# Performance work log

Measured on AMD Instinct MI355X. Metric: run time of the kernel, lower is better.

The kernel has to match this reference:

```python
import jax, jax.numpy as jnp
import numpy as np

D = 64; T = 128; B = 64; R = 20; SEE = 10; H = 4; C = 4
N = 300000; P = 4000; K = 256


def setup_inputs() -> dict:
    key = jax.random.key(0)
    ks = jax.random.split(key, 24)
    g = lambda k, s: jax.random.normal(k, s, dtype=jnp.float32) * 0.05
    return {
        "prob_id": jax.random.randint(ks[0], (T, B), 0, P),
        "skills": jax.random.randint(ks[1], (T, B, C), 0, K),
        "response": jax.random.randint(ks[2], (T, B), 0, 2),
        "bg_index": jax.random.randint(ks[3], (T, B, R), 0, N),
        "mem_prob_ids": jax.random.randint(ks[4], (N,), 0, P),
        "mem_resp": jax.random.randint(ks[5], (N,), 0, 2),
        "mem_concepts": jax.random.randint(ks[6], (N, C), 0, K),
        "states_mem": g(ks[7], (N, D)),
        "concept_emb": g(ks[8], (K - 1, D)),
        "prob_emb": g(ks[9], (P - 1, D)),
        "W_pred": g(ks[10], (9 * D, 1)), "b_pred": jnp.zeros((1,), jnp.float32),
        "W_ih": g(ks[11], (4 * D, 3 * D)), "W_hh": g(ks[12], (D, 3 * D)),
        "b_ih": jnp.zeros((3 * D,), jnp.float32), "b_hh": jnp.zeros((3 * D,), jnp.float32),
        "W_batch": g(ks[13], (H, 3 * D, D)), "b_batch": jnp.zeros((H, D), jnp.float32),
        "W_bg": g(ks[14], (H, 3 * D, D)), "b_bg": jnp.zeros((H, D), jnp.float32),
        "W_bgint": g(ks[15], (6 * D, 6 * D)), "b_bgint": jnp.zeros((6 * D,), jnp.float32),
        "W_hisint": g(ks[16], (2 * D, 6 * D)), "b_hisint": jnp.zeros((6 * D,), jnp.float32),
        "W_inmap": g(ks[17], (10 * D, 4 * D)), "b_inmap": jnp.zeros((4 * D,), jnp.float32),
        "dir_w": g(ks[18], (2, 1)), "heads_map": g(ks[19], (H, 1)),
    }


def _forward(floats, ints):
    (states_mem, concept_emb, prob_emb, W_pred, b_pred, W_ih, W_hh, b_ih, b_hh,
     W_batch, b_batch, W_bg, b_bg, W_bgint, b_bgint, W_hisint, b_hisint,
     W_inmap, b_inmap, dir_w, heads_map) = floats
    prob_id, skills, response, bg_index, mem_prob_ids, mem_resp, mem_concepts = ints
    f32 = states_mem.dtype
    # embedding tables with zero row 0 (padding id)
    prob_cat = jnp.concatenate([jnp.zeros((1, D), f32), prob_emb], axis=0)
    conc_cat = jnp.concatenate([jnp.zeros((1, D), f32), concept_emb], axis=0)

    def prob_rep(pid, sk):
        pr = prob_cat[pid]                                     # [..., D]
        fsum = jnp.sum((sk != 0).astype(f32), axis=-1)
        div = jnp.where(fsum == 0, 1.0, fsum)[..., None]
        mean = jnp.sum(conc_cat[sk], axis=-2) / div            # masked-mean concept emb
        return jnp.concatenate([mean, pr], axis=-1)            # [..., 2D]

    dw = jax.nn.softmax(dir_w, axis=0)                          # [2,1]
    hm = heads_map[:, 0]                                        # [H]

    def step(carry, xt):
        h, h_buf, resp_buf, v_buf, t = carry
        pid, sk, resp, bgi = xt
        respf = resp.astype(f32)
        v = prob_rep(pid, sk)                                   # [B,2D]
        hidden_v = jnp.concatenate([h, v], axis=-1)             # [B,3D]
        bgi = bgi[:, :SEE]                                      # keep first see_ref refs
        bg_h = states_mem[bgi]                                  # [B,S,D] irregular gather
        bg_v = prob_rep(mem_prob_ids[bgi], mem_concepts[bgi])   # [B,S,2D]
        bg_r = mem_resp[bgi].astype(f32)[..., None]             # [B,S,1]
        all_hv = jnp.concatenate([bg_h, bg_v], axis=-1)         # [B,S,3D]
        bg_ctx = jnp.concatenate([all_hv * bg_r, all_hv * (1.0 - bg_r)], axis=-1)  # [B,S,6D]
        # multi-head attention over retrieved background states
        q = jnp.einsum('bk,hkd->bhd', hidden_v, W_batch) + b_batch[None]
        kk = jnp.einsum('bsk,hkd->bhsd', all_hv, W_bg) + b_bg[None, :, None, :]
        att = jax.nn.softmax(jnp.einsum('bhd,bhsd->bhs', q, kk) / np.sqrt(3.0 * D), axis=-1)
        heads = jnp.einsum('bhs,bsk->bhk', att, bg_ctx)          # [B,H,6D]
        bg_atts = jnp.einsum('bhk,h->bk', heads, hm)             # [B,6D]
        # attention over own history (positions 0..t valid)
        rb = resp_buf.astype(f32)[..., None]                     # [B,T+1,1]
        hr_cat = jnp.concatenate([h_buf * rb, h_buf * (1.0 - rb)], axis=-1)  # [B,T+1,2D]
        sc = jnp.einsum('bk,btk->bt', v, v_buf) / np.sqrt(2.0 * D)
        sc = jnp.where(jnp.arange(T + 1)[None, :] <= t, sc, -1e9)
        his_atts = jnp.einsum('bt,btk->bk', jax.nn.softmax(sc, axis=-1), hr_cat)  # [B,2D]
        peer = (bg_atts @ W_bgint + b_bgint) * dw[0, 0] + (his_atts @ W_hisint + b_hisint) * dw[1, 0]
        prob = (jnp.concatenate([peer, v, h], axis=-1) @ W_pred + b_pred)[:, 0]
        v_resp = jnp.concatenate([v * respf[:, None], v * (1.0 - respf[:, None])], axis=-1)
        gru_in = jnp.concatenate([peer, v_resp], axis=-1) @ W_inmap + b_inmap  # [B,4D]
        # GRU cell (torch GRUCell convention)
        gx = gru_in @ W_ih + b_ih
        gh = h @ W_hh + b_hh
        xr, xz, xn = jnp.split(gx, 3, axis=-1)
        hr, hz, hn = jnp.split(gh, 3, axis=-1)
        r = jax.nn.sigmoid(xr + hr)
        z = jax.nn.sigmoid(xz + hz)
        n = jnp.tanh(xn + r * hn)
        new_h = (1.0 - z) * n + z * h
        h_buf = h_buf.at[:, t + 1].set(new_h)
        resp_buf = resp_buf.at[:, t + 1].set(resp.astype(resp_buf.dtype))
        v_buf = v_buf.at[:, t + 1].set(v)
        return (new_h, h_buf, resp_buf, v_buf, t + 1), prob

    init = (jnp.zeros((B, D), f32), jnp.zeros((B, T + 1, D), f32),
            jnp.zeros((B, T + 1), jnp.int32), jnp.zeros((B, T + 1, 2 * D), f32),
            jnp.int32(0))
    xs = (prob_id, skills, response.astype(jnp.int32), bg_index)
    _, probs = jax.lax.scan(step, init, xs)                      # [T,B]
    return probs.T.reshape(-1)                                   # concat over batch, seq_num=T


def reference(prob_id, skills, response, bg_index, mem_prob_ids, mem_resp, mem_concepts,
              states_mem, concept_emb, prob_emb, W_pred, b_pred, W_ih, W_hh, b_ih, b_hh,
              W_batch, b_batch, W_bg, b_bg, W_bgint, b_bgint, W_hisint, b_hisint,
              W_inmap, b_inmap, dir_w, heads_map):
    floats = (states_mem, concept_emb, prob_emb, W_pred, b_pred, W_ih, W_hh, b_ih, b_hh,
              W_batch, b_batch, W_bg, b_bg, W_bgint, b_bgint, W_hisint, b_hisint,
              W_inmap, b_inmap, dir_w, heads_map)
    ints = (prob_id, skills, response, bg_index, mem_prob_ids, mem_resp, mem_concepts)
    return _forward(floats, ints)
```

## Files before the change

### kernel.cpp

```cpp
#include <hip/hip_runtime.h>
#include <hip/hip_bf16.h>

#define TT 128
#define BB 64
#define DD 64
#define RR 20
#define SEE 10
#define HH 4
#define CC 4
#define NITEM (TT*BB*SEE)
typedef __attribute__((ext_vector_type(8))) short short8;
typedef __attribute__((ext_vector_type(4))) float floatx4;

static __device__ __forceinline__ float wave_sum(float v) {
  v += __shfl_xor(v, 32); v += __shfl_xor(v, 16); v += __shfl_xor(v, 8);
  v += __shfl_xor(v, 4);  v += __shfl_xor(v, 2);  v += __shfl_xor(v, 1);
  return v;
}
static __device__ __forceinline__ float wave_max(float v) {
  v = fmaxf(v, __shfl_xor(v, 32)); v = fmaxf(v, __shfl_xor(v, 16)); v = fmaxf(v, __shfl_xor(v, 8));
  v = fmaxf(v, __shfl_xor(v, 4));  v = fmaxf(v, __shfl_xor(v, 2));  v = fmaxf(v, __shfl_xor(v, 1));
  return v;
}
static __device__ __forceinline__ unsigned short f2bf(float x) {
  __hip_bfloat16 h = __float2bfloat16(x);
  return *reinterpret_cast<unsigned short*>(&h);
}
static __device__ __forceinline__ unsigned int pack2(float lo, float hi) {
  return (unsigned int)f2bf(lo) | ((unsigned int)f2bf(hi) << 16);
}
static __device__ __forceinline__ void ldsbar() {
  asm volatile("s_waitcnt lgkmcnt(0)" ::: "memory");
  __builtin_amdgcn_s_barrier();
  asm volatile("" ::: "memory");
}

__global__ void build_v(const int* __restrict__ prob_id, const int* __restrict__ skills,
                        const float* __restrict__ concept_emb, const float* __restrict__ prob_emb,
                        float* __restrict__ V, float* __restrict__ VT) {
  int tb = blockIdx.x; int t = tb >> 6, b = tb & 63; int d = threadIdx.x;
  int pid = prob_id[tb];
  float pr = pid ? prob_emb[(pid - 1) * 64 + d] : 0.0f;
  int cnt = 0; float sum = 0.0f;
#pragma unroll
  for (int c = 0; c < 4; ++c) {
    int sk = skills[tb * 4 + c];
    if (sk) { ++cnt; sum += concept_emb[(sk - 1) * 64 + d]; }
  }
  float mean = sum / (float)(cnt ? cnt : 1);
  V[tb * 128 + d] = mean;
  V[tb * 128 + 64 + d] = pr;
  VT[b * 16384 + d * 128 + t] = mean;
  VT[b * 16384 + (64 + d) * 128 + t] = pr;
}

__global__ __launch_bounds__(256) void gemm_f32(
    const float* __restrict__ A, const float* __restrict__ B, float* __restrict__ C,
    const float* __restrict__ bias, int M, int N, int K,
    int lda, int ldb, int ldc, long sA, long sB, long sC, float scale) {
  __shared__ __align__(16) float As[64 * 36];
  __shared__ __align__(16) float Bs[32 * 64];
  const float* Ab = A + (long)blockIdx.z * sA;
  const float* Bb = B + (long)blockIdx.z * sB;
  float* Cb = C + (long)blockIdx.z * sC;
  int m0 = blockIdx.y * 64, n0 = blockIdx.x * 64;
  int tid = threadIdx.x;
  int ti = tid & 15, tj = tid >> 4;
  float acc[4][4] = {};
  for (int kc = 0; kc < K; kc += 32) {
#pragma unroll
    for (int p = 0; p < 2; ++p) {
      int q = tid + 256 * p;
      int row = q >> 3, kq = q & 7;
      *(float4*)&As[row * 36 + 4 * kq] = *(const float4*)&Ab[(size_t)(m0 + row) * lda + kc + 4 * kq];
    }
#pragma unroll
    for (int p = 0; p < 2; ++p) {
      int q = tid + 256 * p;
      int k = q >> 4, nq = q & 15;
      *(float4*)&Bs[k * 64 + 4 * nq] = *(const float4*)&Bb[(size_t)(kc + k) * ldb + n0 + 4 * nq];
    }
    __syncthreads();
#pragma unroll
    for (int k4 = 0; k4 < 8; ++k4) {
      float4 av[4], bv[4];
#pragma unroll
      for (int m = 0; m < 4; ++m) av[m] = *(const float4*)&As[(ti + 16 * m) * 36 + 4 * k4];
#pragma unroll
      for (int kk = 0; kk < 4; ++kk) bv[kk] = *(const float4*)&Bs[(4 * k4 + kk) * 64 + 4 * tj];
#pragma unroll
      for (int m = 0; m < 4; ++m) {
        const float* ap = (const float*)&av[m];
#pragma unroll
        for (int kk = 0; kk < 4; ++kk) {
          float a = ap[kk];
          acc[m][0] += a * bv[kk].x; acc[m][1] += a * bv[kk].y;
          acc[m][2] += a * bv[kk].z; acc[m][3] += a * bv[kk].w;
        }
      }
    }
    __syncthreads();
  }
  float4 bq = make_float4(0.f, 0.f, 0.f, 0.f);
  if (bias) bq = *(const float4*)&bias[n0 + 4 * tj];
#pragma unroll
  for (int m = 0; m < 4; ++m) {
    int row = m0 + ti + 16 * m;
    float4 o;
    o.x = acc[m][0] * scale + bq.x; o.y = acc[m][1] * scale + bq.y;
    o.z = acc[m][2] * scale + bq.z; o.w = acc[m][3] * scale + bq.w;
    *(float4*)&Cb[(size_t)row * ldc + n0 + 4 * tj] = o;
  }
}

__global__ __launch_bounds__(256) void k_small(
    const float* __restrict__ W_batch, const float* __restrict__ W_bg, const float* __restrict__ b_bg,
    const float* __restrict__ W_bgint, const float* __restrict__ b_bgint,
    const float* __restrict__ W_hisint, const float* __restrict__ b_hisint,
    const float* __restrict__ W_ih, const float* __restrict__ b_ih, const float* __restrict__ b_inmap,
    const float* __restrict__ W_pred, const float* __restrict__ b_pred, const float* __restrict__ dir_w,
    const float* __restrict__ M12, unsigned short* __restrict__ B1T, float* __restrict__ Hmix,
    float* __restrict__ WgT, float* __restrict__ WBvcat, float* __restrict__ Bgxv,
    float* __restrict__ c4, float* __restrict__ cgx, float* __restrict__ uh,
    float* __restrict__ bgp, float* __restrict__ c0, float* __restrict__ dwv) {
  int idx = blockIdx.x * 256 + threadIdx.x;
  const int R0 = 49152, R1 = 86016, R2 = 122880, R3 = 147456, R4 = 196608,
            R5 = 229376, R6 = 278528, R7 = 278784, R8 = 278976, R9 = 279104,
            R10 = 279488, R11 = 279489, R12 = 279491;
  if (idx < R0) {
    int k = idx >> 8, n = idx & 255; int h = n >> 6, i = n & 63;
    float s = 0.f;
    for (int d = 0; d < 64; ++d) s += W_bg[h * 12288 + k * 64 + d] * W_batch[h * 12288 + i * 64 + d];
    B1T[n * 192 + k] = f2bf(s);
  } else if (idx < R1) {
    int r = idx - R0; int k = r / 192, c = r - k * 192;
    float s = 0.f;
    for (int j = 0; j < 384; ++j) s += W_bgint[k * 384 + j] * M12[j * 192 + c];
    B1T[(256 + c) * 192 + k] = f2bf(s);
  } else if (idx < R2) {
    int r = idx - R1; int k = r / 192, c = r - k * 192;
    float s = 0.f;
    for (int j = 0; j < 384; ++j) s += W_bgint[(192 + k) * 384 + j] * M12[j * 192 + c];
    B1T[(448 + c) * 192 + k] = f2bf(s);
  } else if (idx < R3) {
    int r = idx - R2; int i = r / 192, c = r - i * 192;
    float s = 0.f;
    for (int j = 0; j < 384; ++j) s += W_hisint[i * 384 + j] * M12[j * 192 + c];
    Hmix[i * 192 + c] = s;
  } else if (idx < R4) {
    int r = idx - R3; int h = r / 12288; int rem = r - h * 12288; int d = rem / 192, k = rem - d * 192;
    WgT[r] = W_bg[h * 12288 + k * 64 + d];
  } else if (idx < R5) {
    int r = idx - R4; int i = r >> 8, n = r & 255; int h = n >> 6, d = n & 63;
    WBvcat[r] = W_batch[h * 12288 + (64 + i) * 64 + d];
  } else if (idx < R6) {
    int r = idx - R5; int i = r / 384, c = r - i * 384;
    Bgxv[r] = (c < 192) ? M12[(384 + i) * 192 + c] : M12[(512 + i) * 192 + (c - 192)];
  } else if (idx < R7) {
    int n = idx - R6; int h = n >> 6, i = n & 63;
    float s = 0.f;
    for (int d = 0; d < 64; ++d) s += W_batch[h * 12288 + i * 64 + d] * b_bg[h * 64 + d];
    c4[n] = s;
  } else if (idx < R8) {
    int c = idx - R7;
    float e0 = __expf(dir_w[0]), e1 = __expf(dir_w[1]);
    float dw0 = e0 / (e0 + e1), dw1 = e1 / (e0 + e1);
    float s = b_ih[c];
    for (int i = 0; i < 256; ++i) s += b_inmap[i] * W_ih[i * 192 + c];
    for (int k = 0; k < 384; ++k) s += (dw0 * b_bgint[k] + dw1 * b_hisint[k]) * M12[k * 192 + c];
    cgx[c] = s;
  } else if (idx < R9) {
    int i = idx - R8;
    float s = 0.f;
    for (int j = 0; j < 384; ++j) s += W_hisint[i * 384 + j] * W_pred[j];
    uh[i] = s;
  } else if (idx < R10) {
    int k = idx - R9;
    float s = 0.f;
    for (int j = 0; j < 384; ++j) s += W_bgint[k * 384 + j] * W_pred[j];
    bgp[k] = s;
  } else if (idx < R11) {
    float e0 = __expf(dir_w[0]), e1 = __expf(dir_w[1]);
    float dw0 = e0 / (e0 + e1), dw1 = e1 / (e0 + e1);
    float s = b_pred[0];
    for (int k = 0; k < 384; ++k) s += (dw0 * b_bgint[k] + dw1 * b_hisint[k]) * W_pred[k];
    c0[0] = s;
  } else if (idx < R12) {
    float e0 = __expf(dir_w[0]), e1 = __expf(dir_w[1]);
    dwv[idx - R11] = (idx == R11) ? e0 / (e0 + e1) : e1 / (e0 + e1);
  }
}

#define APAD 200
#define BPAD 40
__global__ __launch_bounds__(256) void big_gemm(
    const int* __restrict__ bg_index, const int* __restrict__ mem_prob_ids,
    const int* __restrict__ mem_resp, const int* __restrict__ mem_concepts,
    const float* __restrict__ states_mem, const float* __restrict__ concept_emb,
    const float* __restrict__ prob_emb, const unsigned short* __restrict__ B1T,
    const float* __restrict__ c4, float* __restrict__ P4s, float* __restrict__ Cg) {
  __shared__ unsigned short As[128 * APAD];
  __shared__ unsigned short Bs[128 * BPAD];
  __shared__ int bgi_l[128]; __shared__ int rf_l[128];
  int mt = blockIdx.x;
  int tid = threadIdx.x;
  int lane = tid & 63, wv = tid >> 6;
  if (tid < 128) {
    int item = mt * 128 + tid;
    int t = item / 640; int rem = item - t * 640; int b = rem / 10; int s = rem - b * 10;
    int g = bg_index[(t * 64 + b) * 20 + s];
    bgi_l[tid] = g;
    rf_l[tid] = mem_resp[g];
  }
  __syncthreads();
  {
    int half = lane >> 5;
    int hl = lane & 31;
    for (int rr = 0; rr < 32; rr += 2) {
      int r = wv * 32 + rr + half;
      int g = bgi_l[r];
      float2 sv = *(const float2*)&states_mem[g * 64 + 2 * hl];
      *(unsigned int*)&As[r * APAD + 2 * hl] = pack2(sv.x, sv.y);
      float s0 = 0.f, s1 = 0.f; int cnt = 0;
#pragma unroll
      for (int c = 0; c < 4; ++c) {
        int sk = mem_concepts[g * 4 + c];
        if (sk) { ++cnt; float2 e = *(const float2*)&concept_emb[(sk - 1) * 64 + 2 * hl]; s0 += e.x; s1 += e.y; }
      }
      float inv = 1.0f / (float)(cnt ? cnt : 1);
      *(unsigned int*)&As[r * APAD + 64 + 2 * hl] = pack2(s0 * inv, s1 * inv);
      int pid = mem_prob_ids[g];
      float2 pv = make_float2(0.f, 0.f);
      if (pid) pv = *(const float2*)&prob_emb[(pid - 1) * 64 + 2 * hl];
      *(unsigned int*)&As[r * APAD + 128 + 2 * hl] = pack2(pv.x, pv.y);
    }
  }
  int l15 = lane & 15, q = lane >> 4;
  int mh = (wv & 1) * 64, nh = (wv >> 1) * 64;
  const float invs192 = 0.07216878364870323f;
  for (int nt = 0; nt < 5; ++nt) {
    int n0 = nt * 128;
    floatx4 acc[4][4];
#pragma unroll
    for (int mi = 0; mi < 4; ++mi)
#pragma unroll
      for (int ni = 0; ni < 4; ++ni)
#pragma unroll
        for (int r = 0; r < 4; ++r) acc[mi][ni][r] = 0.f;
    for (int kc = 0; kc < 6; ++kc) {
      __syncthreads();
#pragma unroll
      for (int u = 0; u < 2; ++u) {
        int un = tid * 2 + u;
        int n = un >> 2, kk = (un & 3) * 8;
        *(float4*)&Bs[n * BPAD + kk] = *(const float4*)&B1T[(size_t)(n0 + n) * 192 + kc * 32 + kk];
      }
      __syncthreads();
      short8 a[4], bfr[4];
#pragma unroll
      for (int mi = 0; mi < 4; ++mi)
        a[mi] = *reinterpret_cast<const short8*>(&As[(mh + mi * 16 + l15) * APAD + kc * 32 + q * 8]);
#pragma unroll
      for (int ni = 0; ni < 4; ++ni)
        bfr[ni] = *reinterpret_cast<const short8*>(&Bs[(nh + ni * 16 + l15) * BPAD + q * 8]);
#pragma unroll
      for (int mi = 0; mi < 4; ++mi)
#pragma unroll
        for (int ni = 0; ni < 4; ++ni)
          acc[mi][ni] = __builtin_amdgcn_mfma_f32_16x16x32_bf16(a[mi], bfr[ni], acc[mi][ni], 0, 0, 0);
    }
    float c4v[4];
    if (n0 + nh < 256) {
#pragma unroll
      for (int ni = 0; ni < 4; ++ni) c4v[ni] = c4[n0 + nh + ni * 16 + l15];
    }
#pragma unroll
    for (int mi = 0; mi < 4; ++mi) {
#pragma unroll
      for (int r = 0; r < 4; ++r) {
        int row = mh + mi * 16 + q * 4 + r;
        int item = mt * 128 + row;
        int rf = rf_l[row];
#pragma unroll
        for (int ni = 0; ni < 4; ++ni) {
          int coln = n0 + nh + ni * 16 + l15;
          float o = acc[mi][ni][r];
          if (coln < 256) {
            P4s[(size_t)item * 256 + coln] = (o + c4v[ni]) * invs192;
          } else if (coln < 448) {
            if (rf) Cg[(size_t)item * 192 + (coln - 256)] = o;
          } else {
            if (!rf) Cg[(size_t)item * 192 + (coln - 448)] = o;
          }
        }
      }
    }
  }
}

__global__ __launch_bounds__(256) void k5(
    const int* __restrict__ bg_index, const int* __restrict__ mem_prob_ids,
    const int* __restrict__ mem_resp, const int* __restrict__ mem_concepts,
    const float* __restrict__ states_mem, const float* __restrict__ concept_emb,
    const float* __restrict__ prob_emb, const float* __restrict__ RQ, const float* __restrict__ QV,
    const float* __restrict__ b_bg, const float* __restrict__ bgp, const float* __restrict__ V,
    const float* __restrict__ W_pred, const float* __restrict__ c0,
    float* __restrict__ SQVb, float* __restrict__ cbp, float* __restrict__ PROBC) {
  int tb = blockIdx.x;
  int tid = threadIdx.x;
  int lane = tid & 63, wv = tid >> 6;
  __shared__ float ahv[10 * 196];
  __shared__ float rql[4 * 196];
  __shared__ float bgpl[384];
  __shared__ int bgi_l[10]; __shared__ int rf_s[10];
  __shared__ float cqb[4];
  if (tid < 10) { int g = bg_index[tb * 20 + tid]; bgi_l[tid] = g; rf_s[tid] = mem_resp[g]; }
  for (int i = tid; i < 384; i += 256) bgpl[i] = bgp[i];
  for (int i = tid; i < 768; i += 256) { int h = i / 192, c = i - h * 192; rql[h * 196 + c] = RQ[(size_t)tb * 768 + i]; }
  if (tid < 4) {
    float s = 0.f;
    for (int d = 0; d < 64; ++d) s += QV[tb * 256 + tid * 64 + d] * b_bg[tid * 64 + d];
    cqb[tid] = s;
  }
  __syncthreads();
  for (int s = 0; s < 10; ++s) {
    if (tid < 192) {
      int g = bgi_l[s]; float v;
      if (tid < 64) v = states_mem[g * 64 + tid];
      else if (tid < 128) {
        int d = tid - 64; float sum = 0.f; int cnt = 0;
#pragma unroll
        for (int c = 0; c < 4; ++c) { int sk = mem_concepts[g * 4 + c]; if (sk) { ++cnt; sum += concept_emb[(sk - 1) * 64 + d]; } }
        v = sum / (float)(cnt ? cnt : 1);
      } else {
        int pid = mem_prob_ids[g];
        v = pid ? prob_emb[(pid - 1) * 64 + (tid - 128)] : 0.0f;
      }
      ahv[s * 196 + tid] = v;
    }
  }
  __syncthreads();
  const float invs192 = 0.07216878364870323f;
  for (int q = 0; q < 10; ++q) {
    float v = ahv[q * 196 + lane] * rql[wv * 196 + lane]
            + ahv[q * 196 + 64 + lane] * rql[wv * 196 + 64 + lane]
            + ahv[q * 196 + 128 + lane] * rql[wv * 196 + 128 + lane];
    v = wave_sum(v);
    if (lane == 0) SQVb[tb * 40 + wv * 10 + q] = (v + cqb[wv]) * invs192;
  }
  if (wv == 0) {
    for (int q = 0; q < 10; ++q) {
      int off = rf_s[q] ? 0 : 192;
      float v = ahv[q * 196 + lane] * bgpl[off + lane]
              + ahv[q * 196 + 64 + lane] * bgpl[off + 64 + lane]
              + ahv[q * 196 + 128 + lane] * bgpl[off + 128 + lane];
      v = wave_sum(v);
      if (lane == 0) cbp[tb * 10 + q] = v;
    }
  }
  if (wv == 1) {
    float v = V[tb * 128 + lane] * W_pred[384 + lane] + V[tb * 128 + 64 + lane] * W_pred[448 + lane];
    v = wave_sum(v);
    if (lane == 0) PROBC[tb] = v + c0[0];
  }
}

__global__ __launch_bounds__(64) void prep_pw(const float* S, const int* response,
                                              float* PW, float* PR) {
  int bt = blockIdx.x; int b = bt >> 7, t = bt & 127;
  int lane = threadIdx.x;
  size_t row = (size_t)bt * 128;
  float s0 = (lane == 0) ? 0.f : ((lane <= t) ? S[row + lane - 1] : -1e30f);
  float s1 = (lane + 64 <= t) ? S[row + lane + 63] : -1e30f;
  float m = wave_max(fmaxf(s0, s1));
  float e0 = (lane <= t) ? __expf(s0 - m) : 0.f;
  float e1 = (lane + 64 <= t) ? __expf(s1 - m) : 0.f;
  float inv = 1.f / wave_sum(e0 + e1);
  float r0 = (lane >= 1) ? (float)response[(lane - 1) * 64 + b] : 0.f;
  float r1 = (float)response[(lane + 63) * 64 + b];
  PW[row + lane] = e0 * inv;
  PW[row + 64 + lane] = e1 * inv;
  PR[row + lane] = e0 * inv * r0;
  PR[row + 64 + lane] = e1 * inv * r1;
}

__global__ __launch_bounds__(512) void seq_kernel(
    const int* __restrict__ response, const float* __restrict__ P4s,
    const float* __restrict__ SQVb, const float* __restrict__ Cg,
    const float* __restrict__ GXV, const float* __restrict__ cbp,
    const float* __restrict__ PROBC, const float* __restrict__ PW,
    const float* __restrict__ PR, const float* __restrict__ Hmix,
    const float* __restrict__ W_hh, const float* __restrict__ b_hh,
    const float* __restrict__ cgx, const float* __restrict__ uh,
    const float* __restrict__ W_pred, const float* __restrict__ heads_map,
    const float* __restrict__ dwv, float* __restrict__ out) {
  int b = blockIdx.x;
  int tid = threadIdx.x;
  int lane = tid & 63, wv = tid >> 6;
  int cg3 = lane * 3;
  float hreg[16][3], wreg[8][3];
#pragma unroll
  for (int ii = 0; ii < 16; ++ii)
#pragma unroll
    for (int cc = 0; cc < 3; ++cc) hreg[ii][cc] = Hmix[(wv * 16 + ii) * 192 + cg3 + cc];
#pragma unroll
  for (int ii = 0; ii < 8; ++ii)
#pragma unroll
    for (int cc = 0; cc < 3; ++cc) wreg[ii][cc] = W_hh[(wv * 8 + ii) * 192 + cg3 + cc];
  __shared__ float h_hist[128][64];
  __shared__ __align__(16) float PWl[128];
  __shared__ __align__(16) float PRl[128];
  __shared__ float h_cur[64];
  __shared__ float score_l[40], ws_l[10];
  __shared__ float hisA[128];
  __shared__ float red8[8][128];
  __shared__ float redW[8][192];
  __shared__ float gx_l[192], gh_l[192];
  __shared__ float cgx_l[192], uh_l[128], wph_l[64], hm_l[4];
  __shared__ float sm_mx[4], sm_inv[4];
  __shared__ float phis_s, hwp_s, pbg_s;
  if (tid < 64) { h_cur[tid] = 0.f; h_hist[0][tid] = 0.f; wph_l[tid] = W_pred[512 + tid]; }
  if (tid < 192) cgx_l[tid] = cgx[tid];
  if (tid >= 256 && tid < 384) uh_l[tid - 256] = uh[tid - 256];
  if (tid >= 384 && tid < 388) hm_l[tid - 384] = heads_map[tid - 384];
  float dw0 = dwv[0], dw1 = dwv[1];
  int poff[5];
#pragma unroll
  for (int q = 0; q < 5; ++q) { int p = wv * 5 + q; int hh = p / 10, s = p - hh * 10; poff[q] = s * 256 + hh * 64 + lane; }
  float pf_p4[5];
#pragma unroll
  for (int q = 0; q < 5; ++q) pf_p4[q] = P4s[(size_t)b * 2560 + poff[q]];
  float pf_sqv = 0.f;
  if (lane < 5) pf_sqv = SQVb[b * 40 + wv * 5 + lane];
  float pf_cg[10]; float pf_gxv = 0.f;
  if (tid >= 64 && tid < 256) {
    int c = tid - 64;
#pragma unroll
    for (int s = 0; s < 10; ++s) pf_cg[s] = Cg[(size_t)(b * 10 + s) * 192 + c];
    int rn = response[b];
    pf_gxv = GXV[(size_t)b * 384 + (rn ? 0 : 192) + c];
  } else {
#pragma unroll
    for (int s = 0; s < 10; ++s) pf_cg[s] = 0.f;
  }
  float pf_cbp = 0.f;
  if (wv == 5 && lane < 10) pf_cbp = cbp[b * 10 + lane];
  float pf_probc = 0.f;
  if (tid == 0) pf_probc = PROBC[b];
  float4 pf_pw = make_float4(0.f, 0.f, 0.f, 0.f), pf_pr = pf_pw;
  if (tid < 32) pf_pw = *(const float4*)&PW[((size_t)(b * 128 + 0)) * 128 + 4 * tid];
  else if (tid < 64) pf_pr = *(const float4*)&PR[((size_t)(b * 128 + 0)) * 128 + 4 * (tid - 32)];
  if (tid < 32) *(float4*)&PWl[4 * tid] = pf_pw;
  else if (tid < 64) *(float4*)&PRl[4 * (tid - 32)] = pf_pr;
  if (tid < 32) pf_pw = *(const float4*)&PW[((size_t)(b * 128 + 1)) * 128 + 4 * tid];
  else if (tid < 64) pf_pr = *(const float4*)&PR[((size_t)(b * 128 + 1)) * 128 + 4 * (tid - 32)];
  ldsbar();

  for (int t = 0; t < 128; ++t) {
    int tn = (t < 127) ? t + 1 : 127;
    int tbn = tn * 64 + b;
    float hc = h_cur[lane];
    {
      float v[5];
#pragma unroll
      for (int q = 0; q < 5; ++q) v[q] = hc * pf_p4[q];
#pragma unroll
      for (int d = 32; d; d >>= 1) {
#pragma unroll
        for (int q = 0; q < 5; ++q) v[q] += __shfl_xor(v[q], d);
      }
#pragma unroll
      for (int q = 0; q < 5; ++q) if (lane == q) score_l[wv * 5 + q] = v[q] + pf_sqv;
    }
#pragma unroll
    for (int q = 0; q < 5; ++q) pf_p4[q] = P4s[(size_t)tbn * 2560 + poff[q]];
    if (lane < 5) pf_sqv = SQVb[tbn * 40 + wv * 5 + lane];
    {
      float l0 = 0.f, l1 = 0.f, l2 = 0.f;
#pragma unroll
      for (int ii = 0; ii < 8; ++ii) {
        float hv = h_cur[wv * 8 + ii];
        l0 += hv * wreg[ii][0]; l1 += hv * wreg[ii][1]; l2 += hv * wreg[ii][2];
      }
      redW[wv][cg3] = l0; redW[wv][cg3 + 1] = l1; redW[wv][cg3 + 2] = l2;
    }
    {
      float aR = 0.f, aA = 0.f;
      for (int j = wv; j <= t; j += 8) {
        float w = PWl[j], r = PRl[j], hv = h_hist[j][lane];
        aA += w * hv; aR += r * hv;
      }
      red8[wv][lane] = aR; red8[wv][64 + lane] = aA;
    }
    ldsbar();
    if (tid < 64) {
      float sR = 0.f, sA = 0.f;
#pragma unroll
      for (int g = 0; g < 8; ++g) { sR += red8[g][tid]; sA += red8[g][64 + tid]; }
      hisA[tid] = sR; hisA[64 + tid] = sA - sR;
    } else if (tid < 256) {
      int c = tid - 64; float g = 0.f;
#pragma unroll
      for (int gg = 0; gg < 8; ++gg) g += redW[gg][c];
      gh_l[c] = g + b_hh[c];
    } else if (tid >= 448 && tid < 452) {
      int h = tid - 448;
      float mx = -1e30f;
#pragma unroll
      for (int s = 0; s < 10; ++s) mx = fmaxf(mx, score_l[h * 10 + s]);
      float sum = 0.f;
#pragma unroll
      for (int s = 0; s < 10; ++s) sum += __expf(score_l[h * 10 + s] - mx);
      sm_mx[h] = mx; sm_inv[h] = hm_l[h] / sum;
    }
    ldsbar();
    {
      float l0 = 0.f, l1 = 0.f, l2 = 0.f;
#pragma unroll
      for (int ii = 0; ii < 16; ++ii) {
        float hv = hisA[wv * 16 + ii];
        l0 += hv * hreg[ii][0]; l1 += hv * hreg[ii][1]; l2 += hv * hreg[ii][2];
      }
      redW[wv][cg3] = l0; redW[wv][cg3 + 1] = l1; redW[wv][cg3 + 2] = l2;
    }
    if (tid >= 448 && tid < 458) {
      int s = tid - 448; float w = 0.f;
#pragma unroll
      for (int h = 0; h < 4; ++h) w += sm_inv[h] * __expf(score_l[h * 10 + s] - sm_mx[h]);
      ws_l[s] = w;
    }
    if (wv == 0) {
      float p = hisA[lane] * uh_l[lane] + hisA[64 + lane] * uh_l[64 + lane];
      p = wave_sum(p);
      if (lane == 0) phis_s = p;
    }
    if (wv == 6) {
      float p = hc * wph_l[lane];
      p = wave_sum(p);
      if (lane == 0) hwp_s = p;
    }
    ldsbar();
    if (tid >= 64 && tid < 256) {
      int c = tid - 64;
      float gbg = 0.f;
#pragma unroll
      for (int s = 0; s < 10; ++s) gbg += ws_l[s] * pf_cg[s];
      float gxh = 0.f;
#pragma unroll
      for (int g = 0; g < 8; ++g) gxh += redW[g][c];
      gx_l[c] = dw0 * gbg + dw1 * gxh + pf_gxv + cgx_l[c];
#pragma unroll
      for (int s = 0; s < 10; ++s) pf_cg[s] = Cg[(size_t)(tbn * 10 + s) * 192 + c];
      int rn = response[tbn];
      pf_gxv = GXV[(size_t)tbn * 384 + (rn ? 0 : 192) + c];
    }
    if (wv == 5) {
      float p = (lane < 10) ? ws_l[lane] * pf_cbp : 0.f;
      p = wave_sum(p);
      if (lane == 0) pbg_s = p;
      if (lane < 10) pf_cbp = cbp[tbn * 10 + lane];
    }
    ldsbar();
    if (tid < 64) {
      float xr = gx_l[tid], xz = gx_l[64 + tid], xn = gx_l[128 + tid];
      float hr = gh_l[tid], hz = gh_l[64 + tid], hn = gh_l[128 + tid];
      float r = 1.f / (1.f + __expf(-(xr + hr)));
      float z = 1.f / (1.f + __expf(-(xz + hz)));
      float n = tanhf(xn + r * hn);
      float hnew = (1.f - z) * n + z * h_cur[tid];
      h_cur[tid] = hnew;
      if (t < 127) h_hist[t + 1][tid] = hnew;
    }
    if (tid == 0) {
      out[b * 128 + t] = dw0 * pbg_s + dw1 * phis_s + hwp_s + pf_probc;
      pf_probc = PROBC[tbn];
    }
    if (tid < 32) *(float4*)&PWl[4 * tid] = pf_pw;
    else if (tid < 64) *(float4*)&PRl[4 * (tid - 32)] = pf_pr;
    {
      int rn2 = (t + 2 < 128) ? t + 2 : 127;
      if (tid < 32) pf_pw = *(const float4*)&PW[((size_t)(b * 128 + rn2)) * 128 + 4 * tid];
      else if (tid < 64) pf_pr = *(const float4*)&PR[((size_t)(b * 128 + rn2)) * 128 + 4 * (tid - 32)];
    }
    ldsbar();
  }
}

extern "C" void kernel_launch(void* const* d_in, const int* in_sizes, int n_in,
                              void* d_out, int out_size, void* d_ws, size_t ws_size,
                              hipStream_t stream) {
  const int* prob_id      = (const int*)d_in[0];
  const int* skills       = (const int*)d_in[1];
  const int* response     = (const int*)d_in[2];
  const int* bg_index     = (const int*)d_in[3];
  const int* mem_prob_ids = (const int*)d_in[4];
  const int* mem_resp     = (const int*)d_in[5];
  const int* mem_concepts = (const int*)d_in[6];
  const float* states_mem  = (const float*)d_in[7];
  const float* concept_emb = (const float*)d_in[8];
  const float* prob_emb    = (const float*)d_in[9];
  const float* W_pred   = (const float*)d_in[10];
  const float* b_pred   = (const float*)d_in[11];
  const float* W_ih     = (const float*)d_in[12];
  const float* W_hh     = (const float*)d_in[13];
  const float* b_ih     = (const float*)d_in[14];
  const float* b_hh     = (const float*)d_in[15];
  const float* W_batch  = (const float*)d_in[16];
  const float* b_batch  = (const float*)d_in[17];
  const float* W_bg     = (const float*)d_in[18];
  const float* b_bg     = (const float*)d_in[19];
  const float* W_bgint  = (const float*)d_in[20];
  const float* b_bgint  = (const float*)d_in[21];
  const float* W_hisint = (const float*)d_in[22];
  const float* b_hisint = (const float*)d_in[23];
  const float* W_inmap  = (const float*)d_in[24];
  const float* b_inmap  = (const float*)d_in[25];
  const float* dir_w    = (const float*)d_in[26];
  const float* heads_map= (const float*)d_in[27];
  float* out = (float*)d_out;

  float* w = (float*)d_ws;
  size_t off = 0;
  auto alloc = [&](size_t n) { float* p = w + off; off += (n + 3) & ~(size_t)3; return p; };
  float* M12    = alloc(640 * 192);
  unsigned short* B1T = (unsigned short*)alloc(640 * 192 / 2);
  float* Hmix   = alloc(128 * 192);
  float* WgT    = alloc(4 * 192 * 64);
  float* WBvcat = alloc(128 * 256);
  float* Bgxv   = alloc(128 * 384);
  float* c4     = alloc(256);
  float* cgx    = alloc(192);
  float* uh     = alloc(128);
  float* bgp    = alloc(384);
  float* c0     = alloc(1);
  float* dwv    = alloc(2);
  float* V      = alloc((size_t)8192 * 128);
  float* VT     = alloc((size_t)64 * 128 * 128);
  float* QV     = alloc((size_t)8192 * 256);
  float* RQ     = alloc((size_t)8192 * 768);
  float* GXV    = alloc((size_t)8192 * 384);
  float* S      = alloc((size_t)64 * 128 * 128);
  float* PR     = alloc((size_t)64 * 128 * 128);
  float* P4s    = alloc((size_t)NITEM * 256);
  float* Cg     = alloc((size_t)NITEM * 192);
  float* SQVb   = alloc((size_t)8192 * 40);
  float* cbp    = alloc((size_t)NITEM);
  float* PROBC  = alloc(8192);
  (void)ws_size; (void)in_sizes; (void)n_in; (void)out_size;

  build_v<<<8192, 64, 0, stream>>>(prob_id, skills, concept_emb, prob_emb, V, VT);
  gemm_f32<<<dim3(3, 10, 1), 256, 0, stream>>>(W_inmap, W_ih, M12, nullptr,
      640, 192, 256, 256, 192, 192, 0, 0, 0, 1.0f);
  k_small<<<1092, 256, 0, stream>>>(W_batch, W_bg, b_bg, W_bgint, b_bgint, W_hisint, b_hisint,
      W_ih, b_ih, b_inmap, W_pred, b_pred, dir_w, M12, B1T, Hmix, WgT, WBvcat, Bgxv,
      c4, cgx, uh, bgp, c0, dwv);
  gemm_f32<<<dim3(4, 128, 1), 256, 0, stream>>>(V, WBvcat, QV, b_batch,
      8192, 256, 128, 128, 256, 256, 0, 0, 0, 1.0f);
  gemm_f32<<<dim3(3, 128, 4), 256, 0, stream>>>(QV, WgT, RQ, nullptr,
      8192, 192, 64, 256, 192, 768, 64, 12288, 192, 1.0f);
  gemm_f32<<<dim3(6, 128, 1), 256, 0, stream>>>(V, Bgxv, GXV, nullptr,
      8192, 384, 128, 128, 384, 384, 0, 0, 0, 1.0f);
  gemm_f32<<<dim3(2, 2, 64), 256, 0, stream>>>(V, VT, S, nullptr,
      128, 128, 128, 8192, 128, 128, 128, 16384, 16384, 0.08838834764831845f);
  prep_pw<<<8192, 64, 0, stream>>>(S, response, S, PR);
  big_gemm<<<dim3(640), 256, 0, stream>>>(bg_index, mem_prob_ids, mem_resp, mem_concepts,
      states_mem, concept_emb, prob_emb, B1T, c4, P4s, Cg);
  k5<<<8192, 256, 0, stream>>>(bg_index, mem_prob_ids, mem_resp, mem_concepts,
      states_mem, concept_emb, prob_emb, RQ, QV, b_bg, bgp, V, W_pred, c0, SQVb, cbp, PROBC);
  seq_kernel<<<64, 512, 0, stream>>>(response, P4s, SQVb, Cg, GXV, cbp, PROBC,
      S, PR, Hmix, W_hh, b_hh, cgx, uh, W_pred, heads_map, dwv, out);
}
```

Before: 936.1 us.

## Restructure recurrent GRU step to cut shuffle reductions and rebalance barrier phases

Rewrites the per-timestep loop of the sequential recurrence kernel. Attention scores now come from per-wave partial dot products over 8 hidden elements instead of five 64-lane shuffle reductions, and the softmax max-subtraction is dropped. The h·W_pred and history·uh dot products become per-wave partial sums held in registers. The gx computation is folded into the 64 GRU threads, which removes the gx_l stage, and the prefetch work moves to otherwise idle waves. The aim is less shuffle and serial work on the critical path of each step. The cost is extra registers per thread and exponentials without max subtraction, which could overflow for large scores.

```diff
diff --git a/kernel.cpp b/kernel.cpp
--- a/kernel.cpp
+++ b/kernel.cpp
@@ -407,82 +407,95 @@
   for (int ii = 0; ii < 8; ++ii)
 #pragma unroll
     for (int cc = 0; cc < 3; ++cc) wreg[ii][cc] = W_hh[(wv * 8 + ii) * 192 + cg3 + cc];
+  float wph_reg[8], uh_reg[16];
+  if (lane == 0) {
+#pragma unroll
+    for (int j = 0; j < 8; ++j) wph_reg[j] = W_pred[512 + wv * 8 + j];
+#pragma unroll
+    for (int ii = 0; ii < 16; ++ii) uh_reg[ii] = uh[wv * 16 + ii];
+  }
   __shared__ float h_hist[128][64];
   __shared__ __align__(16) float PWl[128];
   __shared__ __align__(16) float PRl[128];
   __shared__ float h_cur[64];
-  __shared__ float score_l[40], ws_l[10];
+  __shared__ float part_sc[8 * 40];
+  __shared__ float e_l[40];
+  __shared__ float ws_l[10];
+  __shared__ float inv_l[4];
   __shared__ float hisA[128];
   __shared__ float red8[8][128];
-  __shared__ float redW[8][192];
-  __shared__ float gx_l[192], gh_l[192];
-  __shared__ float cgx_l[192], uh_l[128], wph_l[64], hm_l[4];
-  __shared__ float sm_mx[4], sm_inv[4];
-  __shared__ float phis_s, hwp_s, pbg_s;
-  if (tid < 64) { h_cur[tid] = 0.f; h_hist[0][tid] = 0.f; wph_l[tid] = W_pred[512 + tid]; }
+  __shared__ float redWg[8][192];
+  __shared__ float redWh[8][192];
+  __shared__ float gh_l[192];
+  __shared__ float cgx_l[192], hm_l[4];
+  __shared__ float hwp_p[8], phis_p[8];
+  __shared__ float phis_s, hwp_s;
+  if (tid < 64) { h_cur[tid] = 0.f; h_hist[0][tid] = 0.f; }
   if (tid < 192) cgx_l[tid] = cgx[tid];
-  if (tid >= 256 && tid < 384) uh_l[tid - 256] = uh[tid - 256];
   if (tid >= 384 && tid < 388) hm_l[tid - 384] = heads_map[tid - 384];
   float dw0 = dwv[0], dw1 = dwv[1];
-  int poff[5];
-#pragma unroll
-  for (int q = 0; q < 5; ++q) { int p = wv * 5 + q; int hh = p / 10, s = p - hh * 10; poff[q] = s * 256 + hh * 64 + lane; }
-  float pf_p4[5];
-#pragma unroll
-  for (int q = 0; q < 5; ++q) pf_p4[q] = P4s[(size_t)b * 2560 + poff[q]];
+  int sc_off = 0;
+  if (lane < 40) { int hh = lane / 10, s = lane - hh * 10; sc_off = s * 256 + hh * 64 + wv * 8; }
+  float4 pfa = make_float4(0, 0, 0, 0), pfb = pfa;
+  if (lane < 40) {
+    pfa = *(const float4*)&P4s[(size_t)b * 2560 + sc_off];
+    pfb = *(const float4*)&P4s[(size_t)b * 2560 + sc_off + 4];
+  }
   float pf_sqv = 0.f;
-  if (lane < 5) pf_sqv = SQVb[b * 40 + wv * 5 + lane];
-  float pf_cg[10]; float pf_gxv = 0.f;
-  if (tid >= 64 && tid < 256) {
-    int c = tid - 64;
-#pragma unroll
-    for (int s = 0; s < 10; ++s) pf_cg[s] = Cg[(size_t)(b * 10 + s) * 192 + c];
+  if (tid < 40) pf_sqv = SQVb[b * 40 + tid];
+  float pf_cg0[10], pf_cg1[10], pf_cg2[10];
+  float pf_gx0 = 0.f, pf_gx1 = 0.f, pf_gx2 = 0.f;
+  if (tid < 64) {
+#pragma unroll
+    for (int s = 0; s < 10; ++s) {
+      size_t base = (size_t)(b * 10 + s) * 192;
+      pf_cg0[s] = Cg[base + tid]; pf_cg1[s] = Cg[base + 64 + tid]; pf_cg2[s] = Cg[base + 128 + tid];
+    }
     int rn = response[b];
-    pf_gxv = GXV[(size_t)b * 384 + (rn ? 0 : 192) + c];
-  } else {
-#pragma unroll
-    for (int s = 0; s < 10; ++s) pf_cg[s] = 0.f;
-  }
-  float pf_cbp = 0.f;
-  if (wv == 5 && lane < 10) pf_cbp = cbp[b * 10 + lane];
-  float pf_probc = 0.f;
-  if (tid == 0) pf_probc = PROBC[b];
-  float4 pf_pw = make_float4(0.f, 0.f, 0.f, 0.f), pf_pr = pf_pw;
-  if (tid < 32) pf_pw = *(const float4*)&PW[((size_t)(b * 128 + 0)) * 128 + 4 * tid];
-  else if (tid < 64) pf_pr = *(const float4*)&PR[((size_t)(b * 128 + 0)) * 128 + 4 * (tid - 32)];
-  if (tid < 32) *(float4*)&PWl[4 * tid] = pf_pw;
-  else if (tid < 64) *(float4*)&PRl[4 * (tid - 32)] = pf_pr;
-  if (tid < 32) pf_pw = *(const float4*)&PW[((size_t)(b * 128 + 1)) * 128 + 4 * tid];
-  else if (tid < 64) pf_pr = *(const float4*)&PR[((size_t)(b * 128 + 1)) * 128 + 4 * (tid - 32)];
+    size_t gb = (size_t)b * 384 + (rn ? 0 : 192);
+    pf_gx0 = GXV[gb + tid]; pf_gx1 = GXV[gb + 64 + tid]; pf_gx2 = GXV[gb + 128 + tid];
+  }
+  float pf_cbp[10]; float pf_probc = 0.f;
+  if (tid == 448) {
+#pragma unroll
+    for (int s = 0; s < 10; ++s) pf_cbp[s] = cbp[b * 10 + s];
+    pf_probc = PROBC[b];
+  }
+  float4 pf_pw = make_float4(0, 0, 0, 0), pf_pr = pf_pw;
+  if (tid >= 128 && tid < 160) pf_pw = *(const float4*)&PW[((size_t)(b * 128 + 0)) * 128 + 4 * (tid - 128)];
+  else if (tid >= 160 && tid < 192) pf_pr = *(const float4*)&PR[((size_t)(b * 128 + 0)) * 128 + 4 * (tid - 160)];
+  if (tid >= 128 && tid < 160) *(float4*)&PWl[4 * (tid - 128)] = pf_pw;
+  else if (tid >= 160 && tid < 192) *(float4*)&PRl[4 * (tid - 160)] = pf_pr;
+  if (tid >= 128 && tid < 160) pf_pw = *(const float4*)&PW[((size_t)(b * 128 + 1)) * 128 + 4 * (tid - 128)];
+  else if (tid >= 160 && tid < 192) pf_pr = *(const float4*)&PR[((size_t)(b * 128 + 1)) * 128 + 4 * (tid - 160)];
   ldsbar();
 
   for (int t = 0; t < 128; ++t) {
     int tn = (t < 127) ? t + 1 : 127;
     int tbn = tn * 64 + b;
-    float hc = h_cur[lane];
-    {
-      float v[5];
-#pragma unroll
-      for (int q = 0; q < 5; ++q) v[q] = hc * pf_p4[q];
-#pragma unroll
-      for (int d = 32; d; d >>= 1) {
-#pragma unroll
-        for (int q = 0; q < 5; ++q) v[q] += __shfl_xor(v[q], d);
-      }
-#pragma unroll
-      for (int q = 0; q < 5; ++q) if (lane == q) score_l[wv * 5 + q] = v[q] + pf_sqv;
-    }
-#pragma unroll
-    for (int q = 0; q < 5; ++q) pf_p4[q] = P4s[(size_t)tbn * 2560 + poff[q]];
-    if (lane < 5) pf_sqv = SQVb[tbn * 40 + wv * 5 + lane];
+    float h_l[8];
+#pragma unroll
+    for (int j = 0; j < 8; ++j) h_l[j] = h_cur[wv * 8 + j];
+    if (lane < 40) {
+      float v = h_l[0] * pfa.x + h_l[1] * pfa.y + h_l[2] * pfa.z + h_l[3] * pfa.w
+              + h_l[4] * pfb.x + h_l[5] * pfb.y + h_l[6] * pfb.z + h_l[7] * pfb.w;
+      part_sc[wv * 40 + lane] = v;
+      pfa = *(const float4*)&P4s[(size_t)tbn * 2560 + sc_off];
+      pfb = *(const float4*)&P4s[(size_t)tbn * 2560 + sc_off + 4];
+    }
     {
       float l0 = 0.f, l1 = 0.f, l2 = 0.f;
 #pragma unroll
       for (int ii = 0; ii < 8; ++ii) {
-        float hv = h_cur[wv * 8 + ii];
-        l0 += hv * wreg[ii][0]; l1 += hv * wreg[ii][1]; l2 += hv * wreg[ii][2];
-      }
-      redW[wv][cg3] = l0; redW[wv][cg3 + 1] = l1; redW[wv][cg3 + 2] = l2;
+        l0 += h_l[ii] * wreg[ii][0]; l1 += h_l[ii] * wreg[ii][1]; l2 += h_l[ii] * wreg[ii][2];
+      }
+      redWg[wv][cg3] = l0; redWg[wv][cg3 + 1] = l1; redWg[wv][cg3 + 2] = l2;
+    }
+    if (lane == 0) {
+      float hp = 0.f;
+#pragma unroll
+      for (int j = 0; j < 8; ++j) hp += h_l[j] * wph_reg[j];
+      hwp_p[wv] = hp;
     }
     {
       float aR = 0.f, aA = 0.f;
@@ -493,76 +506,83 @@
       red8[wv][lane] = aR; red8[wv][64 + lane] = aA;
     }
     ldsbar();
-    if (tid < 64) {
+    if (tid < 40) {
+      float s = pf_sqv;
+#pragma unroll
+      for (int w = 0; w < 8; ++w) s += part_sc[w * 40 + tid];
+      e_l[tid] = __expf(s);
+      pf_sqv = SQVb[tbn * 40 + tid];
+    } else if (tid >= 64 && tid < 128) {
+      int i = tid - 64;
       float sR = 0.f, sA = 0.f;
 #pragma unroll
-      for (int g = 0; g < 8; ++g) { sR += red8[g][tid]; sA += red8[g][64 + tid]; }
-      hisA[tid] = sR; hisA[64 + tid] = sA - sR;
-    } else if (tid < 256) {
-      int c = tid - 64; float g = 0.f;
-#pragma unroll
-      for (int gg = 0; gg < 8; ++gg) g += redW[gg][c];
+      for (int g = 0; g < 8; ++g) { sR += red8[g][i]; sA += red8[g][64 + i]; }
+      hisA[i] = sR; hisA[64 + i] = sA - sR;
+    } else if (tid >= 256 && tid < 448) {
+      int c = tid - 256; float g = 0.f;
+#pragma unroll
+      for (int gg = 0; gg < 8; ++gg) g += redWg[gg][c];
       gh_l[c] = g + b_hh[c];
-    } else if (tid >= 448 && tid < 452) {
-      int h = tid - 448;
-      float mx = -1e30f;
-#pragma unroll
-      for (int s = 0; s < 10; ++s) mx = fmaxf(mx, score_l[h * 10 + s]);
-      float sum = 0.f;
-#pragma unroll
-      for (int s = 0; s < 10; ++s) sum += __expf(score_l[h * 10 + s] - mx);
-      sm_mx[h] = mx; sm_inv[h] = hm_l[h] / sum;
+    } else if (tid == 450) {
+      float s = 0.f;
+#pragma unroll
+      for (int g = 0; g < 8; ++g) s += hwp_p[g];
+      hwp_s = s;
     }
     ldsbar();
     {
+      float hA[16];
+#pragma unroll
+      for (int ii = 0; ii < 16; ++ii) hA[ii] = hisA[wv * 16 + ii];
       float l0 = 0.f, l1 = 0.f, l2 = 0.f;
 #pragma unroll
       for (int ii = 0; ii < 16; ++ii) {
-        float hv = hisA[wv * 16 + ii];
-        l0 += hv * hreg[ii][0]; l1 += hv * hreg[ii][1]; l2 += hv * hreg[ii][2];
-      }
-      redW[wv][cg3] = l0; redW[wv][cg3 + 1] = l1; redW[wv][cg3 + 2] = l2;
-    }
-    if (tid >= 448 && tid < 458) {
-      int s = tid - 448; float w = 0.f;
-#pragma unroll
-      for (int h = 0; h < 4; ++h) w += sm_inv[h] * __expf(score_l[h * 10 + s] - sm_mx[h]);
+        l0 += hA[ii] * hreg[ii][0]; l1 += hA[ii] * hreg[ii][1]; l2 += hA[ii] * hreg[ii][2];
+      }
+      redWh[wv][cg3] = l0; redWh[wv][cg3 + 1] = l1; redWh[wv][cg3 + 2] = l2;
+      if (lane == 0) {
+        float pp = 0.f;
+#pragma unroll
+        for (int ii = 0; ii < 16; ++ii) pp += hA[ii] * uh_reg[ii];
+        phis_p[wv] = pp;
+      }
+    }
+    if (tid >= 452 && tid < 456) {
+      int h = tid - 452;
+      float den = 0.f;
+#pragma unroll
+      for (int s = 0; s < 10; ++s) den += e_l[h * 10 + s];
+      inv_l[h] = hm_l[h] / den;
+    }
+    ldsbar();
+    if (tid >= 256 && tid < 266) {
+      int s = tid - 256;
+      float w = 0.f;
+#pragma unroll
+      for (int h = 0; h < 4; ++h) w += inv_l[h] * e_l[h * 10 + s];
       ws_l[s] = w;
-    }
-    if (wv == 0) {
-      float p = hisA[lane] * uh_l[lane] + hisA[64 + lane] * uh_l[64 + lane];
-      p = wave_sum(p);
-      if (lane == 0) phis_s = p;
-    }
-    if (wv == 6) {
-      float p = hc * wph_l[lane];
-      p = wave_sum(p);
-      if (lane == 0) hwp_s = p;
-    }
-    ldsbar();
-    if (tid >= 64 && tid < 256) {
-      int c = tid - 64;
-      float gbg = 0.f;
-#pragma unroll
-      for (int s = 0; s < 10; ++s) gbg += ws_l[s] * pf_cg[s];
-      float gxh = 0.f;
-#pragma unroll
-      for (int g = 0; g < 8; ++g) gxh += redW[g][c];
-      gx_l[c] = dw0 * gbg + dw1 * gxh + pf_gxv + cgx_l[c];
-#pragma unroll
-      for (int s = 0; s < 10; ++s) pf_cg[s] = Cg[(size_t)(tbn * 10 + s) * 192 + c];
-      int rn = response[tbn];
-      pf_gxv = GXV[(size_t)tbn * 384 + (rn ? 0 : 192) + c];
-    }
-    if (wv == 5) {
-      float p = (lane < 10) ? ws_l[lane] * pf_cbp : 0.f;
-      p = wave_sum(p);
-      if (lane == 0) pbg_s = p;
-      if (lane < 10) pf_cbp = cbp[tbn * 10 + lane];
+    } else if (tid == 266) {
+      float p = 0.f;
+#pragma unroll
+      for (int g = 0; g < 8; ++g) p += phis_p[g];
+      phis_s = p;
     }
     ldsbar();
     if (tid < 64) {
-      float xr = gx_l[tid], xz = gx_l[64 + tid], xn = gx_l[128 + tid];
+      float gxh0 = 0.f, gxh1 = 0.f, gxh2 = 0.f;
+#pragma unroll
+      for (int g = 0; g < 8; ++g) {
+        gxh0 += redWh[g][tid]; gxh1 += redWh[g][64 + tid]; gxh2 += redWh[g][128 + tid];
+      }
+      float gbg0 = 0.f, gbg1 = 0.f, gbg2 = 0.f;
+#pragma unroll
+      for (int s = 0; s < 10; ++s) {
+        float w = ws_l[s];
+        gbg0 += w * pf_cg0[s]; gbg1 += w * pf_cg1[s]; gbg2 += w * pf_cg2[s];
+      }
+      float xr = dw0 * gbg0 + dw1 * gxh0 + pf_gx0 + cgx_l[tid];
+      float xz = dw0 * gbg1 + dw1 * gxh1 + pf_gx1 + cgx_l[64 + tid];
+      float xn = dw0 * gbg2 + dw1 * gxh2 + pf_gx2 + cgx_l[128 + tid];
       float hr = gh_l[tid], hz = gh_l[64 + tid], hn = gh_l[128 + tid];
       float r = 1.f / (1.f + __expf(-(xr + hr)));
       float z = 1.f / (1.f + __expf(-(xz + hz)));
@@ -570,17 +590,28 @@
       float hnew = (1.f - z) * n + z * h_cur[tid];
       h_cur[tid] = hnew;
       if (t < 127) h_hist[t + 1][tid] = hnew;
-    }
-    if (tid == 0) {
-      out[b * 128 + t] = dw0 * pbg_s + dw1 * phis_s + hwp_s + pf_probc;
+#pragma unroll
+      for (int s = 0; s < 10; ++s) {
+        size_t base = (size_t)(tbn * 10 + s) * 192;
+        pf_cg0[s] = Cg[base + tid]; pf_cg1[s] = Cg[base + 64 + tid]; pf_cg2[s] = Cg[base + 128 + tid];
+      }
+      int rn = response[tbn];
+      size_t gb = (size_t)tbn * 384 + (rn ? 0 : 192);
+      pf_gx0 = GXV[gb + tid]; pf_gx1 = GXV[gb + 64 + tid]; pf_gx2 = GXV[gb + 128 + tid];
+    } else if (tid == 448) {
+      float pbg = 0.f;
+#pragma unroll
+      for (int s = 0; s < 10; ++s) pbg += ws_l[s] * pf_cbp[s];
+      out[b * 128 + t] = dw0 * pbg + dw1 * phis_s + hwp_s + pf_probc;
+#pragma unroll
+      for (int s = 0; s < 10; ++s) pf_cbp[s] = cbp[tbn * 10 + s];
       pf_probc = PROBC[tbn];
-    }
-    if (tid < 32) *(float4*)&PWl[4 * tid] = pf_pw;
-    else if (tid < 64) *(float4*)&PRl[4 * (tid - 32)] = pf_pr;
-    {
+    } else if (tid >= 128 && tid < 192) {
+      if (tid < 160) *(float4*)&PWl[4 * (tid - 128)] = pf_pw;
+      else *(float4*)&PRl[4 * (tid - 160)] = pf_pr;
       int rn2 = (t + 2 < 128) ? t + 2 : 127;
-      if (tid < 32) pf_pw = *(const float4*)&PW[((size_t)(b * 128 + rn2)) * 128 + 4 * tid];
-      else if (tid < 64) pf_pr = *(const float4*)&PR[((size_t)(b * 128 + rn2)) * 128 + 4 * (tid - 32)];
+      if (tid < 160) pf_pw = *(const float4*)&PW[((size_t)(b * 128 + rn2)) * 128 + 4 * (tid - 128)];
+      else pf_pr = *(const float4*)&PR[((size_t)(b * 128 + rn2)) * 128 + 4 * (tid - 160)];
     }
     ldsbar();
   }
```

After: 872.7 us. -6.8%, faster.
